# Performance work log

Measured on AMD Instinct MI355X. Metric: run time of the kernel, lower is better.

## Reference

```python
import jax, jax.numpy as jnp
import numpy as np

HEATMAP_RADIUS = 40.0
OFFSET_RADIUS = 40.0


def setup_inputs() -> dict:
    key = jax.random.key(0)
    k1, k2 = jax.random.split(key)
    feature_maps = jax.random.normal(k1, (4, 57, 512, 512), dtype=jnp.float32)
    landmarks = jax.random.uniform(k2, (4, 19, 2), dtype=jnp.float32)
    return {"feature_maps": feature_maps, "landmarks": landmarks}


def reference(feature_maps, landmarks):
    # feature_maps: [B, 3N, H, W]; landmarks: [B, N, 2] normalized in [0,1)
    B, C, H, W = feature_maps.shape
    N = C // 3
    dt = feature_maps.dtype

    # landmarks * [h, w] then truncation to int (torch .long()); positive so floor == trunc
    scale = jnp.array([H, W], dtype=landmarks.dtype)
    xy = (landmarks * scale).astype(jnp.int32)
    x = xy[..., 0][:, :, None, None]  # [B,N,1,1] row-center
    y = xy[..., 1][:, :, None, None]  # [B,N,1,1] col-center

    ii = jnp.arange(H, dtype=jnp.int32)[:, None]   # [H,1]
    jj = jnp.arange(W, dtype=jnp.int32)[None, :]   # [1,W]

    # Cropping general_heatmap[h-x : 2h-x, w-y : 2w-y] is equivalent to evaluating
    # the disc / linear ramps centered at (x, y):
    di = (ii - x).astype(dt)                       # [B,N,H,1]
    dj = (jj - y).astype(dt)                       # [B,N,1,W]
    dist = jnp.sqrt(di * di + dj * dj)             # [B,N,H,W]
    heatmap = (dist <= HEATMAP_RADIUS).astype(dt)  # [B,N,H,W]
    offmap_x = -di / OFFSET_RADIUS                 # (x - i)/r, [B,N,H,1]
    offmap_y = -dj / OFFSET_RADIUS                 # (y - j)/r, [B,N,1,W]

    logits = feature_maps[:, :N]        # [B,N,H,W]
    pred_x = feature_maps[:, N:2 * N]
    pred_y = feature_maps[:, 2 * N:]

    # Stable BCE-with-logits, mean over H*W per (b, n)
    bce = jnp.maximum(logits, 0) - logits * heatmap + jnp.log1p(jnp.exp(-jnp.abs(logits)))
    bce = jnp.mean(bce, axis=(2, 3))    # [B,N]

    # Masked L1: mean over pixels inside the heatmap disc (count varies near borders)
    cnt = jnp.sum(heatmap, axis=(2, 3))  # [B,N]
    l1x = jnp.sum(jnp.abs(pred_x - offmap_x) * heatmap, axis=(2, 3)) / cnt
    l1y = jnp.sum(jnp.abs(pred_y - offmap_y) * heatmap, axis=(2, 3)) / cnt

    loss = jnp.mean(2.0 * bce + l1x + l1y)
    return loss
```

## Files before the change

kernel.cpp:

```cpp
#include <hip/hip_runtime.h>
#include <math.h>

#define BB 4
#define NN 19
#define CC 57
#define HH 512
#define WW 512
#define HWPIX (HH * WW)
#define RADIUS2 1600.0f
#define ROWS_PER_BLOCK 8

__global__ void zero_ws(float* ws) {
    int t = threadIdx.x;
    if (t < BB * NN * 4) ws[t] = 0.0f;
}

__global__ __launch_bounds__(256) void hm_loss_main(
    const float* __restrict__ fm, const float* __restrict__ lm,
    float* __restrict__ ws)
{
    const int bn = blockIdx.y;
    const int b  = bn / NN;
    const int n  = bn % NN;
    const int row0 = blockIdx.x * ROWS_PER_BLOCK;

    const float lx = lm[(b * NN + n) * 2 + 0];
    const float ly = lm[(b * NN + n) * 2 + 1];
    const int x = (int)(lx * (float)HH);
    const int y = (int)(ly * (float)WW);

    const float* __restrict__ logit = fm + (size_t)(b * CC + n)          * HWPIX;
    const float* __restrict__ predx = fm + (size_t)(b * CC + NN + n)     * HWPIX;
    const float* __restrict__ predy = fm + (size_t)(b * CC + 2 * NN + n) * HWPIX;

    float s_bce = 0.0f, s_cnt = 0.0f, s_l1x = 0.0f, s_l1y = 0.0f;

    const int iters = ROWS_PER_BLOCK * WW / 256;
    #pragma unroll
    for (int it = 0; it < iters; ++it) {
        int idx = it * 256 + threadIdx.x;
        int i = row0 + (idx >> 9);
        int j = idx & (WW - 1);
        int off = i * WW + j;

        float l = logit[off];
        float di = (float)(i - x);
        float dj = (float)(j - y);
        float d2 = di * di + dj * dj;
        bool in = (d2 <= RADIUS2);
        float h = in ? 1.0f : 0.0f;

        s_bce += fmaxf(l, 0.0f) - l * h + log1pf(expf(-fabsf(l)));

        if (in) {
            s_cnt += 1.0f;
            float px = predx[off];
            float py = predy[off];
            s_l1x += fabsf(px + di * (1.0f / 40.0f));
            s_l1y += fabsf(py + dj * (1.0f / 40.0f));
        }
    }

    #pragma unroll
    for (int o = 32; o > 0; o >>= 1) {
        s_bce += __shfl_down(s_bce, o);
        s_cnt += __shfl_down(s_cnt, o);
        s_l1x += __shfl_down(s_l1x, o);
        s_l1y += __shfl_down(s_l1y, o);
    }

    __shared__ float red[4][4];
    int wave = threadIdx.x >> 6;
    int lane = threadIdx.x & 63;
    if (lane == 0) {
        red[wave][0] = s_bce;
        red[wave][1] = s_cnt;
        red[wave][2] = s_l1x;
        red[wave][3] = s_l1y;
    }
    __syncthreads();
    if (threadIdx.x == 0) {
        float a = red[0][0] + red[1][0] + red[2][0] + red[3][0];
        float c = red[0][1] + red[1][1] + red[2][1] + red[3][1];
        float px = red[0][2] + red[1][2] + red[2][2] + red[3][2];
        float py = red[0][3] + red[1][3] + red[2][3] + red[3][3];
        atomicAdd(&ws[bn * 4 + 0], a);
        atomicAdd(&ws[bn * 4 + 1], c);
        atomicAdd(&ws[bn * 4 + 2], px);
        atomicAdd(&ws[bn * 4 + 3], py);
    }
}

__global__ __launch_bounds__(128) void hm_loss_final(
    const float* __restrict__ ws, float* __restrict__ out)
{
    int t = threadIdx.x;
    float term = 0.0f;
    if (t < BB * NN) {
        float bce = ws[t * 4 + 0] * (1.0f / (float)HWPIX);
        float cnt = ws[t * 4 + 1];
        float l1x = ws[t * 4 + 2] / cnt;
        float l1y = ws[t * 4 + 3] / cnt;
        term = 2.0f * bce + l1x + l1y;
    }
    #pragma unroll
    for (int o = 32; o > 0; o >>= 1) term += __shfl_down(term, o);

    __shared__ float red[2];
    if ((t & 63) == 0) red[t >> 6] = term;
    __syncthreads();
    if (t == 0) out[0] = (red[0] + red[1]) * (1.0f / (float)(BB * NN));
}

extern "C" void kernel_launch(void* const* d_in, const int* in_sizes, int n_in,
                              void* d_out, int out_size, void* d_ws, size_t ws_size,
                              hipStream_t stream) {
    const float* fm = (const float*)d_in[0];
    const float* lm = (const float*)d_in[1];
    float* ws  = (float*)d_ws;
    float* out = (float*)d_out;

    zero_ws<<<1, 512, 0, stream>>>(ws);
    dim3 grid(HH / ROWS_PER_BLOCK, BB * NN);
    hm_loss_main<<<grid, 256, 0, stream>>>(fm, lm, ws);
    hm_loss_final<<<1, 128, 0, stream>>>(ws, out);
}
```

Before: 333.7 us.

## Vectorize loads with float4, use fast exp/log, replace atomics with partial buffer

Result: faster. 293.9 us (-11.9%).

```diff
diff --git a/kernel.cpp b/kernel.cpp
--- a/kernel.cpp
+++ b/kernel.cpp
@@ -9,55 +9,79 @@
 #define HWPIX (HH * WW)
 #define RADIUS2 1600.0f
 #define ROWS_PER_BLOCK 8
+#define CHUNKS (HH / ROWS_PER_BLOCK)
+#define VEC_PER_ROW (WW / 4)
 
-__global__ void zero_ws(float* ws) {
-    int t = threadIdx.x;
-    if (t < BB * NN * 4) ws[t] = 0.0f;
-}
 
-__global__ __launch_bounds__(256) void hm_loss_main(
+__global__ __launch_bounds__(256) void hm_main(
     const float* __restrict__ fm, const float* __restrict__ lm,
-    float* __restrict__ ws)
+    float4* __restrict__ part)
 {
     const int bn = blockIdx.y;
     const int b  = bn / NN;
     const int n  = bn % NN;
-    const int row0 = blockIdx.x * ROWS_PER_BLOCK;
+    const int chunk = blockIdx.x;
+    const int row0  = chunk * ROWS_PER_BLOCK;
 
-    const float lx = lm[(b * NN + n) * 2 + 0];
-    const float ly = lm[(b * NN + n) * 2 + 1];
-    const int x = (int)(lx * (float)HH);
-    const int y = (int)(ly * (float)WW);
+    const float lx = lm[bn * 2 + 0];
+    const float ly = lm[bn * 2 + 1];
+    const int x = (int)(lx * 512.0f);
+    const int y = (int)(ly * 512.0f);
 
-    const float* __restrict__ logit = fm + (size_t)(b * CC + n)          * HWPIX;
-    const float* __restrict__ predx = fm + (size_t)(b * CC + NN + n)     * HWPIX;
-    const float* __restrict__ predy = fm + (size_t)(b * CC + 2 * NN + n) * HWPIX;
+    const float4* __restrict__ logit =
+        (const float4*)(fm + (size_t)(b * CC + n) * HWPIX) + row0 * VEC_PER_ROW;
+    const float4* __restrict__ predx =
+        (const float4*)(fm + (size_t)(b * CC + NN + n) * HWPIX) + row0 * VEC_PER_ROW;
+    const float4* __restrict__ predy =
+        (const float4*)(fm + (size_t)(b * CC + 2 * NN + n) * HWPIX) + row0 * VEC_PER_ROW;
 
     float s_bce = 0.0f, s_cnt = 0.0f, s_l1x = 0.0f, s_l1y = 0.0f;
 
-    const int iters = ROWS_PER_BLOCK * WW / 256;
     #pragma unroll
-    for (int it = 0; it < iters; ++it) {
-        int idx = it * 256 + threadIdx.x;
-        int i = row0 + (idx >> 9);
-        int j = idx & (WW - 1);
-        int off = i * WW + j;
+    for (int it = 0; it < 4; ++it) {
+        int v  = it * 256 + threadIdx.x;
+        int r  = v >> 7;
+        int c4 = v & (VEC_PER_ROW - 1);
+        int i  = row0 + r;
+        float di = (float)(i - x);
+        float di2 = di * di;
 
-        float l = logit[off];
-        float di = (float)(i - x);
-        float dj = (float)(j - y);
-        float d2 = di * di + dj * dj;
-        bool in = (d2 <= RADIUS2);
-        float h = in ? 1.0f : 0.0f;
+        float4 l4 = logit[v];
+        float lv[4] = { l4.x, l4.y, l4.z, l4.w };
 
-        s_bce += fmaxf(l, 0.0f) - l * h + log1pf(expf(-fabsf(l)));
+        float djv[4];
+        bool  inm[4];
+        bool  any = false;
+        #pragma unroll
+        for (int e = 0; e < 4; ++e) {
+            float dj = (float)(c4 * 4 + e - y);
+            djv[e] = dj;
+            float d2 = fmaf(dj, dj, di2);
+            inm[e] = (d2 <= RADIUS2);
+            any |= inm[e];
+        }
 
-        if (in) {
-            s_cnt += 1.0f;
-            float px = predx[off];
-            float py = predy[off];
-            s_l1x += fabsf(px + di * (1.0f / 40.0f));
-            s_l1y += fabsf(py + dj * (1.0f / 40.0f));
+        #pragma unroll
+        for (int e = 0; e < 4; ++e) {
+            float l = lv[e];
+            float a = fabsf(l);
+            float sp = __logf(1.0f + __expf(-a));
+            s_bce += fmaxf(l, 0.0f) - (inm[e] ? l : 0.0f) + sp;
+        }
+
+        if (any) {
+            float4 px4 = predx[v];
+            float4 py4 = predy[v];
+            float pxv[4] = { px4.x, px4.y, px4.z, px4.w };
+            float pyv[4] = { py4.x, py4.y, py4.z, py4.w };
+            #pragma unroll
+            for (int e = 0; e < 4; ++e) {
+                if (inm[e]) {
+                    s_cnt += 1.0f;
+                    s_l1x += fabsf(fmaf(di,     0.025f, pxv[e]));
+                    s_l1y += fabsf(fmaf(djv[e], 0.025f, pyv[e]));
+                }
+            }
         }
     }
 
@@ -80,36 +104,43 @@
     }
     __syncthreads();
     if (threadIdx.x == 0) {
-        float a = red[0][0] + red[1][0] + red[2][0] + red[3][0];
-        float c = red[0][1] + red[1][1] + red[2][1] + red[3][1];
-        float px = red[0][2] + red[1][2] + red[2][2] + red[3][2];
-        float py = red[0][3] + red[1][3] + red[2][3] + red[3][3];
-        atomicAdd(&ws[bn * 4 + 0], a);
-        atomicAdd(&ws[bn * 4 + 1], c);
-        atomicAdd(&ws[bn * 4 + 2], px);
-        atomicAdd(&ws[bn * 4 + 3], py);
+        float4 p;
+        p.x = red[0][0] + red[1][0] + red[2][0] + red[3][0];
+        p.y = red[0][1] + red[1][1] + red[2][1] + red[3][1];
+        p.z = red[0][2] + red[1][2] + red[2][2] + red[3][2];
+        p.w = red[0][3] + red[1][3] + red[2][3] + red[3][3];
+        part[bn * CHUNKS + chunk] = p;
     }
 }
 
-__global__ __launch_bounds__(128) void hm_loss_final(
-    const float* __restrict__ ws, float* __restrict__ out)
+__global__ __launch_bounds__(256) void hm_final(
+    const float4* __restrict__ part, float* __restrict__ out)
 {
     int t = threadIdx.x;
-    float term = 0.0f;
-    if (t < BB * NN) {
-        float bce = ws[t * 4 + 0] * (1.0f / (float)HWPIX);
-        float cnt = ws[t * 4 + 1];
-        float l1x = ws[t * 4 + 2] / cnt;
-        float l1y = ws[t * 4 + 3] / cnt;
-        term = 2.0f * bce + l1x + l1y;
+    int wave = t >> 6;
+    int lane = t & 63;
+    float acc = 0.0f;
+
+    #pragma unroll
+    for (int k = 0; k < 19; ++k) {
+        int bn = wave * 19 + k;
+        float4 p = part[bn * CHUNKS + lane];
+        float pb = p.x, pc = p.y, p1 = p.z, p2 = p.w;
+        #pragma unroll
+        for (int o = 32; o > 0; o >>= 1) {
+            pb += __shfl_down(pb, o);
+            pc += __shfl_down(pc, o);
+            p1 += __shfl_down(p1, o);
+            p2 += __shfl_down(p2, o);
+        }
+        if (lane == 0)
+            acc += 2.0f * (pb * (1.0f / (float)HWPIX)) + p1 / pc + p2 / pc;
     }
-    #pragma unroll
-    for (int o = 32; o > 0; o >>= 1) term += __shfl_down(term, o);
 
-    __shared__ float red[2];
-    if ((t & 63) == 0) red[t >> 6] = term;
+    __shared__ float red[4];
+    if (lane == 0) red[wave] = acc;
     __syncthreads();
-    if (t == 0) out[0] = (red[0] + red[1]) * (1.0f / (float)(BB * NN));
+    if (t == 0) out[0] = (red[0] + red[1] + red[2] + red[3]) * (1.0f / (float)(BB * NN));
 }
 
 extern "C" void kernel_launch(void* const* d_in, const int* in_sizes, int n_in,
@@ -117,11 +148,10 @@
                               hipStream_t stream) {
     const float* fm = (const float*)d_in[0];
     const float* lm = (const float*)d_in[1];
-    float* ws  = (float*)d_ws;
+    float4* part = (float4*)d_ws;
     float* out = (float*)d_out;
 
-    zero_ws<<<1, 512, 0, stream>>>(ws);
-    dim3 grid(HH / ROWS_PER_BLOCK, BB * NN);
-    hm_loss_main<<<grid, 256, 0, stream>>>(fm, lm, ws);
-    hm_loss_final<<<1, 128, 0, stream>>>(ws, out);
+    dim3 grid(CHUNKS, BB * NN);
+    hm_main<<<grid, 256, 0, stream>>>(fm, lm, part);
+    hm_final<<<1, 256, 0, stream>>>(part, out);
 }
```
